# Performance work log

Measured on AMD Instinct MI355X. Metric: run time of the kernel, lower is better.

Reference implementation:

```python
import jax, jax.numpy as jnp
import numpy as np

B, SEQ, D, H, E = 4, 4096, 1024, 4096, 8
CAPACITY = 2.0  # k = int(S * capacity) token-expert slots


def setup_inputs() -> dict:
    key = jax.random.key(0)
    ks = jax.random.split(key, 5)
    x = jax.random.normal(ks[0], (B, SEQ, D), dtype=jnp.float32)
    gate_weight = jax.random.normal(ks[1], (E, D), dtype=jnp.float32) * 0.006
    expert_bias = jnp.ones((E, 1), dtype=jnp.float32)
    W1 = jax.random.normal(ks[2], (E, D, H), dtype=jnp.float32) * 0.02
    b1 = jnp.zeros((E, H), dtype=jnp.float32)
    W2 = jax.random.normal(ks[3], (E, H, D), dtype=jnp.float32) * 0.02
    b2 = jnp.zeros((E, D), dtype=jnp.float32)
    return {"x": x, "gate_weight": gate_weight, "expert_bias": expert_bias,
            "W1": W1, "b1": b1, "W2": W2, "b2": b2}


def reference(x, gate_weight, expert_bias, W1, b1, W2, b2):
    Bv, s, Dv = x.shape
    xf = x.reshape(-1, Dv)               # [S, D]
    S = xf.shape[0]
    k = int(S * CAPACITY)

    # router: bias_sigmoid -> scores[e, s] = sigmoid(x @ gate.T + bias)
    logits = jnp.einsum('sd,ed->es', xf, gate_weight) + expert_bias  # [E, S]
    scores = jax.nn.sigmoid(logits)

    # global top-k over flattened (E*S) token-expert pairs
    value, index = jax.lax.top_k(scores.reshape(-1), k)
    index_expert = index // S
    index_token = index % S

    # combine weights: gating score at selected slots, 0 elsewhere (topk indices unique)
    C = jnp.zeros((E * S,), dtype=scores.dtype).at[index].set(value).reshape(E, S)

    token_each_expert = jax.ops.segment_sum(
        jnp.ones((k,), dtype=jnp.float32), index_expert, num_segments=E) / float(k)

    # per-expert MLP, gated combine (tokens with C==0 contribute exactly 0,
    # matching the torch gather/MLP/index_add_ path)
    out = jnp.zeros_like(xf)
    for e in range(E):
        h = jax.nn.gelu(xf @ W1[e] + b1[e], approximate=True)  # [S, H]
        y = h @ W2[e] + b2[e]                                  # [S, D]
        out = out + C[e][:, None] * y

    x_out = out.reshape(Bv, s, Dv)
    return x_out, token_each_expert, jnp.ones((E,), dtype=scores.dtype)
```

## Files before the change

kernel.cpp:

```cpp
#include <hip/hip_runtime.h>
#include <hip/hip_bf16.h>
#include <cstdint>
#include <cstdio>
#include <math.h>

#define S_TOK 16384
#define E_EXP 8
#define DDIM  1024
#define HDIM  4096
#define K_SEL 32768
#define ES    131072
#define OUT_XO 16777216

#define WS_META    0x000000u
#define WS_HIST    0x000100u
#define WS_COUNTS  0x001100u
#define WS_EXOFF   0x001200u
#define WS_TIEIDX  0x001300u
#define WS_CLEAR   0x00A000u
#define WS_TOK     0x010000u
#define WS_COEF    0x090000u
#define WS_SCORES  0x110000u
#define WS_TCNT    0x190000u
#define WS_TSLOT   0x1A0000u
#define WS_XB      0x400000u
#define WS_W1T    0x2400000u
#define WS_W2T    0x6400000u
#define WS_HBUF   0xA400000u
#define WS_TOTAL  0x1A400000u
#define WS_YBUF   WS_W1T

typedef __attribute__((ext_vector_type(4))) float f32x4;
typedef __attribute__((ext_vector_type(8))) short bf16x8;

__device__ __forceinline__ void gload_lds16(const void* g, void* l) {
  __builtin_amdgcn_global_load_lds((const __attribute__((address_space(1))) void*)g,
                                   (__attribute__((address_space(3))) void*)l, 16, 0, 0);
}

__device__ __forceinline__ float gelu_f(float x) {
  float u = __builtin_fmaf(x * x * x, 0.044715f, x);
  float e = __builtin_amdgcn_exp2f(-2.302207976f * u);
  return x * __builtin_amdgcn_rcpf(1.0f + e);
}

#define ABUF0 0
#define ABUF1 32768
#define BBUF0 65536
#define BBUF1 98304
#define HALF  16384

#define PH_BAR() __builtin_amdgcn_s_barrier()
#define VMC0M()  asm volatile("s_waitcnt vmcnt(0)" ::: "memory")
#define VMCN(N)  asm volatile("s_waitcnt vmcnt(" #N ")" ::: "memory")

#define STAGE_A(DST, KE) do { \
  gload_lds16(aS00 + (KE), lds + (DST) + w * 2048); \
  gload_lds16(aS01 + (KE), lds + (DST) + w * 2048 + 1024); \
  gload_lds16(aS10 + (KE), lds + (DST) + HALF + w * 2048); \
  gload_lds16(aS11 + (KE), lds + (DST) + HALF + w * 2048 + 1024); } while (0)
#define STAGE_B(DST, KE) do { \
  gload_lds16(bS00 + (KE), lds + (DST) + w * 2048); \
  gload_lds16(bS01 + (KE), lds + (DST) + w * 2048 + 1024); \
  gload_lds16(bS10 + (KE), lds + (DST) + HALF + w * 2048); \
  gload_lds16(bS11 + (KE), lds + (DST) + HALF + w * 2048 + 1024); } while (0)

#define LDS_A03(AB) { _Pragma("unroll") for (int ii = 0; ii < 4; ii++) { \
  a03[ii][0] = *(const bf16x8*)(lds + (AB) + arow + ii * 2048 + pc0); \
  a03[ii][1] = *(const bf16x8*)(lds + (AB) + arow + ii * 2048 + pc1); } }
#define LDS_A47(AB) { _Pragma("unroll") for (int ii = 0; ii < 4; ii++) { \
  a47[ii][0] = *(const bf16x8*)(lds + (AB) + arow + (4 + ii) * 2048 + pc0); \
  a47[ii][1] = *(const bf16x8*)(lds + (AB) + arow + (4 + ii) * 2048 + pc1); } }
#define LDS_B01(BB) { _Pragma("unroll") for (int jj = 0; jj < 2; jj++) { \
  b01[jj][0] = *(const bf16x8*)(lds + (BB) + brow + jj * 2048 + pc0); \
  b01[jj][1] = *(const bf16x8*)(lds + (BB) + brow + jj * 2048 + pc1); } }
#define LDS_B23(BB) { _Pragma("unroll") for (int jj = 0; jj < 2; jj++) { \
  b23[jj][0] = *(const bf16x8*)(lds + (BB) + brow + (2 + jj) * 2048 + pc0); \
  b23[jj][1] = *(const bf16x8*)(lds + (BB) + brow + (2 + jj) * 2048 + pc1); } }

#define MF(AA, BF, IL, JL) { _Pragma("unroll") for (int ii = 0; ii < 4; ii++) \
  _Pragma("unroll") for (int jj = 0; jj < 2; jj++) { \
    acc[(IL)+ii][(JL)+jj] = __builtin_amdgcn_mfma_f32_16x16x32_bf16(AA[ii][0], BF[jj][0], acc[(IL)+ii][(JL)+jj], 0, 0, 0); \
    acc[(IL)+ii][(JL)+jj] = __builtin_amdgcn_mfma_f32_16x16x32_bf16(AA[ii][1], BF[jj][1], acc[(IL)+ii][(JL)+jj], 0, 0, 0); } }

#define TILE(T, AB, BB, ABn, BBn, STGA, STGB, NB, NA) do { \
  PH_BAR(); \
  LDS_A03(AB); \
  if (STGA) STAGE_A(ABn, ((T) + 1) * 64); \
  __builtin_amdgcn_s_setprio(1); MF(a03, b01, 0, 0); MF(a03, b23, 0, 2); __builtin_amdgcn_s_setprio(0); \
  PH_BAR(); \
  LDS_A47(AB); \
  if (STGB) STAGE_B(BB, ((T) + 2) * 64); \
  __builtin_amdgcn_s_setprio(1); MF(a47, b01, 4, 0); __builtin_amdgcn_s_setprio(0); \
  VMCN(NB); \
  LDS_B01(BBn); \
  __builtin_amdgcn_s_setprio(1); MF(a47, b23, 4, 2); __builtin_amdgcn_s_setprio(0); \
  LDS_B23(BBn); \
  VMCN(NA); \
} while (0)

#define TILE_LAST(AB, BB) do { \
  PH_BAR(); \
  LDS_A03(AB); \
  __builtin_amdgcn_s_setprio(1); MF(a03, b01, 0, 0); MF(a03, b23, 0, 2); __builtin_amdgcn_s_setprio(0); \
  PH_BAR(); \
  LDS_A47(AB); \
  __builtin_amdgcn_s_setprio(1); MF(a47, b01, 4, 0); MF(a47, b23, 4, 2); __builtin_amdgcn_s_setprio(0); \
} while (0)

__global__ __launch_bounds__(256) void transpose_bf16_kernel(
    const float* __restrict__ in, __hip_bfloat16* __restrict__ outp, int R, int C)
{
  __shared__ __hip_bfloat16 t[64][66];
  const int c0 = blockIdx.x * 64, r0 = blockIdx.y * 64;
  const size_t eoff = (size_t)blockIdx.z * (size_t)R * (size_t)C;
  const int tx = threadIdx.x & 15, ty = threadIdx.x >> 4;
  const float* ip = in + eoff + (size_t)r0 * C + c0;
#pragma unroll
  for (int i = 0; i < 4; i++) {
    const int r = ty + i * 16;
    float4 v = *(const float4*)(ip + (size_t)r * C + tx * 4);
    t[r][tx * 4 + 0] = __float2bfloat16(v.x);
    t[r][tx * 4 + 1] = __float2bfloat16(v.y);
    t[r][tx * 4 + 2] = __float2bfloat16(v.z);
    t[r][tx * 4 + 3] = __float2bfloat16(v.w);
  }
  __syncthreads();
  __hip_bfloat16* op = outp + eoff + (size_t)c0 * R + r0;
#pragma unroll
  for (int i = 0; i < 4; i++) {
    const int c = ty + i * 16;
    ushort4 u;
    u.x = *(const unsigned short*)&t[tx * 4 + 0][c];
    u.y = *(const unsigned short*)&t[tx * 4 + 1][c];
    u.z = *(const unsigned short*)&t[tx * 4 + 2][c];
    u.w = *(const unsigned short*)&t[tx * 4 + 3][c];
    *(ushort4*)(op + (size_t)c * R + tx * 4) = u;
  }
}

__global__ __launch_bounds__(256) void router_kernel(
    const float* __restrict__ x, const float* __restrict__ gw, const float* __restrict__ bias,
    float* __restrict__ scores, __hip_bfloat16* __restrict__ xb, unsigned* __restrict__ hist0)
{
  __shared__ float g[E_EXP * DDIM];
  __shared__ float bs[E_EXP];
  __shared__ unsigned h0[256];
  const int tid = threadIdx.x;
  for (int i = tid; i < E_EXP * DDIM; i += 256) g[i] = gw[i];
  if (tid < E_EXP) bs[tid] = bias[tid];
  h0[tid] = 0;
  __syncthreads();
  const int w = tid >> 6, lane = tid & 63;
  const int s = blockIdx.x * 4 + w;
  double acc[E_EXP] = {0, 0, 0, 0, 0, 0, 0, 0};
  const float* xrow = x + (size_t)s * DDIM;
  __hip_bfloat16* xbrow = xb + (size_t)s * DDIM;
#pragma unroll 4
  for (int j = 0; j < 16; j++) {
    int d = lane + 64 * j;
    float xv = xrow[d];
    xbrow[d] = __float2bfloat16(xv);
#pragma unroll
    for (int e = 0; e < E_EXP; e++) acc[e] += (double)xv * (double)g[e * DDIM + d];
  }
#pragma unroll
  for (int e = 0; e < E_EXP; e++) {
    double a = acc[e];
#pragma unroll
    for (int off = 32; off > 0; off >>= 1) a += __shfl_xor(a, off);
    acc[e] = a;
  }
  if (lane == 0) {
#pragma unroll
    for (int e = 0; e < E_EXP; e++) {
      double lg = acc[e] + (double)bs[e];
      float sc = (float)(1.0 / (1.0 + exp(-lg)));
      scores[(size_t)e * S_TOK + s] = sc;
      atomicAdd(&h0[__float_as_uint(sc) >> 24], 1u);
    }
  }
  __syncthreads();
  if (h0[tid]) atomicAdd(&hist0[tid], h0[tid]);
}

__global__ __launch_bounds__(256) void hist_pass_kernel(
    const float* __restrict__ scores, const unsigned* __restrict__ meta,
    unsigned* __restrict__ hist, int pass)
{
  __shared__ unsigned h[256];
  const int tid = threadIdx.x;
  h[tid] = 0;
  __syncthreads();
  const unsigned prefix = meta[0];
  const int pshift = 32 - 8 * pass;
  const int bshift = 24 - 8 * pass;
  const unsigned base = blockIdx.x * 2048 + tid;
#pragma unroll
  for (int i = 0; i < 8; i++) {
    unsigned b = __float_as_uint(scores[base + i * 256]);
    bool ok = ((b >> pshift) == prefix);
    if (ok) atomicAdd(&h[(b >> bshift) & 0xFFu], 1u);
  }
  __syncthreads();
  if (h[tid]) atomicAdd(&hist[tid], h[tid]);
}

__global__ __launch_bounds__(256) void scan_pass_kernel(
    const unsigned* __restrict__ hist, unsigned* __restrict__ meta, int final)
{
  const int t = threadIdx.x;
  const unsigned v = hist[t];
  const unsigned prefix = meta[0];
  const unsigned above = meta[1];
  __shared__ unsigned csum[256];
  csum[t] = v;
  __syncthreads();
  for (int off = 1; off < 256; off <<= 1) {
    unsigned add = (t + off < 256) ? csum[t + off] : 0u;
    __syncthreads();
    csum[t] += add;
    __syncthreads();
  }
  const unsigned cge = csum[t];
  const unsigned cgt = cge - v;
  if (above + cgt < K_SEL && above + cge >= K_SEL) {
    meta[0] = (prefix << 8) | (unsigned)t;
    meta[1] = above + cgt;
    if (final) {
      meta[2] = (prefix << 8) | (unsigned)t;
      meta[4] = K_SEL - (above + cgt);
    }
  }
}

__global__ __launch_bounds__(256) void sel_kernel(const float* __restrict__ scores,
                                                  unsigned* __restrict__ meta,
                                                  unsigned* __restrict__ counts,
                                                  int* __restrict__ tok_list,
                                                  float* __restrict__ coef_list,
                                                  unsigned* __restrict__ tie_idx,
                                                  unsigned* __restrict__ tcnt,
                                                  unsigned* __restrict__ tslot)
{
  __shared__ unsigned lcnt[E_EXP], lbase[E_EXP];
  const int tid = threadIdx.x;
  if (tid < E_EXP) lcnt[tid] = 0;
  __syncthreads();
  const unsigned i = blockIdx.x * 256 + tid;
  const float v = scores[i];
  const unsigned b = __float_as_uint(v);
  const unsigned t = meta[2];
  const bool sel = (b > t);
  const unsigned e = i >> 14;
  unsigned myslot = 0;
  if (sel) myslot = atomicAdd(&lcnt[e], 1u);
  else if (b == t) {
    unsigned ts = atomicAdd(&meta[5], 1u);
    if (ts < 8192u) tie_idx[ts] = i;
  }
  __syncthreads();
  if (tid < E_EXP) lbase[tid] = atomicAdd(&counts[tid], lcnt[tid]);
  __syncthreads();
  if (sel) {
    const unsigned slot = lbase[e] + myslot;
    const unsigned p = e * S_TOK + slot;
    const unsigned tok = i & 16383u;
    tok_list[p] = (int)tok;
    coef_list[p] = v;
    unsigned us = atomicAdd(&tcnt[tok], 1u);
    tslot[tok * 8u + us] = (e << 14) | slot;
  }
}

__global__ __launch_bounds__(256) void fin_kernel(const unsigned* __restrict__ meta,
                                                  const unsigned* __restrict__ tie_idx,
                                                  unsigned* __restrict__ counts,
                                                  int* __restrict__ tok_list,
                                                  float* __restrict__ coef_list,
                                                  unsigned* __restrict__ tcnt,
                                                  unsigned* __restrict__ tslot,
                                                  unsigned* __restrict__ exoff,
                                                  float* __restrict__ tail)
{
  unsigned tcnt_ties = meta[5]; if (tcnt_ties > 8192u) tcnt_ties = 8192u;
  const unsigned q = meta[4];
  const float tval = __uint_as_float(meta[2]);
  for (unsigned t = threadIdx.x; t < tcnt_ties; t += 256) {
    unsigned idx = tie_idx[t];
    unsigned rank = 0;
    for (unsigned u = 0; u < tcnt_ties; u++) rank += (tie_idx[u] < idx) ? 1u : 0u;
    if (rank < q) {
      const unsigned e = idx >> 14;
      const unsigned tok = idx & 16383u;
      const unsigned slot = atomicAdd(&counts[e], 1u);
      tok_list[e * S_TOK + slot] = (int)tok;
      coef_list[e * S_TOK + slot] = tval;
      unsigned us = atomicAdd(&tcnt[tok], 1u);
      tslot[tok * 8u + us] = (e << 14) | slot;
    }
  }
  __syncthreads();
  if (threadIdx.x == 0) {
    unsigned o = 0;
    for (int e = 0; e < E_EXP; e++) { exoff[e] = o; o += counts[e]; }
    exoff[E_EXP] = o;
  }
  if (threadIdx.x < E_EXP) {
    tail[threadIdx.x] = (float)counts[threadIdx.x] * (1.0f / (float)K_SEL);
    tail[E_EXP + threadIdx.x] = 1.0f;
  }
}

__global__ __launch_bounds__(512, 1) void gemm1_kernel(
    const __hip_bfloat16* __restrict__ xb,
    const __hip_bfloat16* __restrict__ w1t,
    const float* __restrict__ b1,
    const int* __restrict__ tok_list,
    const unsigned* __restrict__ counts,
    const unsigned* __restrict__ exoff,
    __hip_bfloat16* __restrict__ hbuf)
{
  const int id = blockIdx.x;
  const int L = (id & 7) * 1024 + (id >> 3);
  const int e = L >> 10;
  const int rem = L & 1023;
  const int cnt = (int)counts[e];
  const int m0 = (rem >> 4) * 256;
  if (m0 >= cnt) return;
  const int n0 = (rem & 15) * 256;

  __shared__ __align__(16) char lds[131072];
  __shared__ int s_tok[256];

  const int tid = threadIdx.x;
  const int w = tid >> 6, lane = tid & 63;
  const int wm = w >> 2, wn = w & 3;

  if (tid < 256) {
    int mi = m0 + tid;
    s_tok[tid] = tok_list[e * S_TOK + (mi < cnt ? mi : cnt - 1)];
  }
  __syncthreads();

  const int srl0 = w * 16 + (lane >> 3);
  const int srl1 = srl0 + 8;
  const int gch = ((lane & 7) ^ (lane >> 3)) * 8;
  const __hip_bfloat16* aS00 = xb + (size_t)s_tok[srl0] * DDIM + gch;
  const __hip_bfloat16* aS01 = xb + (size_t)s_tok[srl1] * DDIM + gch;
  const __hip_bfloat16* aS10 = xb + (size_t)s_tok[128 + srl0] * DDIM + gch;
  const __hip_bfloat16* aS11 = xb + (size_t)s_tok[128 + srl1] * DDIM + gch;
  const __hip_bfloat16* w1e = w1t + (size_t)e * HDIM * DDIM;
  const __hip_bfloat16* bS00 = w1e + (size_t)(n0 + srl0) * DDIM + gch;
  const __hip_bfloat16* bS01 = w1e + (size_t)(n0 + srl1) * DDIM + gch;
  const __hip_bfloat16* bS10 = w1e + (size_t)(n0 + 128 + srl0) * DDIM + gch;
  const __hip_bfloat16* bS11 = w1e + (size_t)(n0 + 128 + srl1) * DDIM + gch;

  const int arow = (wm * 128 + (lane & 15)) * 128;
  const int brow = (wn * 64 + (lane & 15)) * 128;
  const int pc0 = (((lane >> 4)) ^ (lane & 7)) * 16;
  const int pc1 = (((lane >> 4) + 4) ^ (lane & 7)) * 16;

  f32x4 acc[8][4] = {};
  bf16x8 a03[4][2], a47[4][2], b01[2][2], b23[2][2];

  STAGE_A(ABUF0, 0);
  STAGE_B(BBUF0, 0);
  STAGE_B(BBUF1, 64);
  VMC0M();
  PH_BAR();
  LDS_B01(BBUF0); LDS_B23(BBUF0);

  const int NKT = DDIM / 64;
  int kt = 0;
  for (; kt + 2 < NKT; kt += 2) {
    TILE(kt,     ABUF0, BBUF0, ABUF1, BBUF1, true, true, 8, 4);
    TILE(kt + 1, ABUF1, BBUF1, ABUF0, BBUF0, true, true, 8, 4);
  }
  TILE(kt, ABUF0, BBUF0, ABUF1, BBUF1, true, false, 4, 0);
  TILE_LAST(ABUF1, BBUF1);
  __syncthreads();

  __hip_bfloat16* stg = (__hip_bfloat16*)lds;
  const float* b1e = b1 + (size_t)e * HDIM;
  float bvj[4];
#pragma unroll
  for (int j = 0; j < 4; j++) bvj[j] = b1e[n0 + wn * 64 + j * 16 + (lane & 15)];
  const int pbase = (int)exoff[e] + m0;

#pragma unroll
  for (int P = 0; P < 4; P++) {
    __syncthreads();
    if (wm == (P >> 1)) {
      const int ib = (P & 1) * 4;
#pragma unroll
      for (int ii = 0; ii < 4; ii++)
#pragma unroll
        for (int jj = 0; jj < 4; jj++)
#pragma unroll
          for (int r = 0; r < 4; r++) {
            const int rloc = ii * 16 + (lane >> 4) * 4 + r;
            const int col = wn * 64 + jj * 16 + (lane & 15);
            stg[rloc * 264 + col] = __float2bfloat16(gelu_f(acc[ib + ii][jj][r] + bvj[jj]));
          }
    }
    __syncthreads();
    const int rr = tid >> 3;
    const int m = P * 64 + rr;
    if (m0 + m < cnt) {
      __hip_bfloat16* dst = hbuf + (size_t)(pbase + m) * HDIM + n0;
      const __hip_bfloat16* src = stg + rr * 264;
#pragma unroll
      for (int c = 0; c < 4; c++)
        *(uint4*)(dst + (tid & 7) * 8 + c * 64) = *(const uint4*)(src + (tid & 7) * 8 + c * 64);
    }
  }
}

__global__ __launch_bounds__(512, 1) void gemm2_kernel(
    const __hip_bfloat16* __restrict__ hbuf,
    const __hip_bfloat16* __restrict__ w2t,
    const float* __restrict__ b2,
    const float* __restrict__ coef_list,
    const unsigned* __restrict__ counts,
    const unsigned* __restrict__ exoff,
    __hip_bfloat16* __restrict__ ybuf)
{
  const int id = blockIdx.x;
  const int L = (id & 7) * 256 + (id >> 3);
  const int e = L >> 8;
  const int rem = L & 255;
  const int cnt = (int)counts[e];
  const int m0 = (rem >> 2) * 256;
  if (m0 >= cnt) return;
  const int n0 = (rem & 3) * 256;

  __shared__ __align__(16) char lds[131072];
  __shared__ float s_coef[256];

  const int tid = threadIdx.x;
  const int w = tid >> 6, lane = tid & 63;
  const int wm = w >> 2, wn = w & 3;
  const int pb = (int)exoff[e];

  if (tid < 256) {
    int mi = m0 + tid;
    s_coef[tid] = (mi < cnt) ? coef_list[e * S_TOK + mi] : 0.0f;
  }
  __syncthreads();

  const int srl0 = w * 16 + (lane >> 3);
  const int srl1 = srl0 + 8;
  const int gch = ((lane & 7) ^ (lane >> 3)) * 8;
  const int ra0 = pb + ((m0 + srl0 < cnt) ? m0 + srl0 : cnt - 1);
  const int ra1 = pb + ((m0 + srl1 < cnt) ? m0 + srl1 : cnt - 1);
  const int ra2 = pb + ((m0 + 128 + srl0 < cnt) ? m0 + 128 + srl0 : cnt - 1);
  const int ra3 = pb + ((m0 + 128 + srl1 < cnt) ? m0 + 128 + srl1 : cnt - 1);
  const __hip_bfloat16* aS00 = hbuf + (size_t)ra0 * HDIM + gch;
  const __hip_bfloat16* aS01 = hbuf + (size_t)ra1 * HDIM + gch;
  const __hip_bfloat16* aS10 = hbuf + (size_t)ra2 * HDIM + gch;
  const __hip_bfloat16* aS11 = hbuf + (size_t)ra3 * HDIM + gch;
  const __hip_bfloat16* w2e = w2t + (size_t)e * DDIM * HDIM;
  const __hip_bfloat16* bS00 = w2e + (size_t)(n0 + srl0) * HDIM + gch;
  const __hip_bfloat16* bS01 = w2e + (size_t)(n0 + srl1) * HDIM + gch;
  const __hip_bfloat16* bS10 = w2e + (size_t)(n0 + 128 + srl0) * HDIM + gch;
  const __hip_bfloat16* bS11 = w2e + (size_t)(n0 + 128 + srl1) * HDIM + gch;

  const int arow = (wm * 128 + (lane & 15)) * 128;
  const int brow = (wn * 64 + (lane & 15)) * 128;
  const int pc0 = (((lane >> 4)) ^ (lane & 7)) * 16;
  const int pc1 = (((lane >> 4) + 4) ^ (lane & 7)) * 16;

  f32x4 acc[8][4] = {};
  bf16x8 a03[4][2], a47[4][2], b01[2][2], b23[2][2];

  STAGE_A(ABUF0, 0);
  STAGE_B(BBUF0, 0);
  STAGE_B(BBUF1, 64);
  VMC0M();
  PH_BAR();
  LDS_B01(BBUF0); LDS_B23(BBUF0);

  const int NKT = HDIM / 64;
  int kt = 0;
  for (; kt + 2 < NKT; kt += 2) {
    TILE(kt,     ABUF0, BBUF0, ABUF1, BBUF1, true, true, 8, 4);
    TILE(kt + 1, ABUF1, BBUF1, ABUF0, BBUF0, true, true, 8, 4);
  }
  TILE(kt, ABUF0, BBUF0, ABUF1, BBUF1, true, false, 4, 0);
  TILE_LAST(ABUF1, BBUF1);
  __syncthreads();

  __hip_bfloat16* stg = (__hip_bfloat16*)lds;
  const float* b2e = b2 + (size_t)e * DDIM;
  float bvj[4];
#pragma unroll
  for (int j = 0; j < 4; j++) bvj[j] = b2e[n0 + wn * 64 + j * 16 + (lane & 15)];
  const int pbase = pb + m0;

#pragma unroll
  for (int P = 0; P < 4; P++) {
    __syncthreads();
    if (wm == (P >> 1)) {
      const int ib = (P & 1) * 4;
#pragma unroll
      for (int ii = 0; ii < 4; ii++)
#pragma unroll
        for (int jj = 0; jj < 4; jj++)
#pragma unroll
          for (int r = 0; r < 4; r++) {
            const int rloc = ii * 16 + (lane >> 4) * 4 + r;
            const int col = wn * 64 + jj * 16 + (lane & 15);
            const float cf = s_coef[P * 64 + rloc];
            stg[rloc * 264 + col] = __float2bfloat16(cf * (acc[ib + ii][jj][r] + bvj[jj]));
          }
    }
    __syncthreads();
    const int rr = tid >> 3;
    const int m = P * 64 + rr;
    if (m0 + m < cnt) {
      __hip_bfloat16* dst = ybuf + (size_t)(pbase + m) * DDIM + n0;
      const __hip_bfloat16* src = stg + rr * 264;
#pragma unroll
      for (int c = 0; c < 4; c++)
        *(uint4*)(dst + (tid & 7) * 8 + c * 64) = *(const uint4*)(src + (tid & 7) * 8 + c * 64);
    }
  }
}

__global__ __launch_bounds__(256) void combine_kernel(
    const __hip_bfloat16* __restrict__ ybuf,
    const unsigned* __restrict__ tcnt,
    const unsigned* __restrict__ tslot,
    const unsigned* __restrict__ exoff,
    float* __restrict__ out)
{
  const int tid = threadIdx.x;
  const int t = blockIdx.x * 2 + (tid >> 7);
  const int d0 = (tid & 127) * 8;
  float a[8] = {0, 0, 0, 0, 0, 0, 0, 0};
  const unsigned n = tcnt[t];
  for (unsigned s = 0; s < n; s++) {
    const unsigned code = tslot[t * 8u + s];
    const unsigned p = exoff[code >> 14] + (code & 16383u);
    bf16x8 v = *(const bf16x8*)(ybuf + (size_t)p * DDIM + d0);
#pragma unroll
    for (int k = 0; k < 8; k++)
      a[k] += __uint_as_float(((unsigned)(unsigned short)v[k]) << 16);
  }
  float* op = out + (size_t)t * DDIM + d0;
  *(float4*)op = make_float4(a[0], a[1], a[2], a[3]);
  *(float4*)(op + 4) = make_float4(a[4], a[5], a[6], a[7]);
}

extern "C" void kernel_launch(void* const* d_in, const int* in_sizes, int n_in,
                              void* d_out, int out_size, void* d_ws, size_t ws_size,
                              hipStream_t stream) {
  const float* x    = (const float*)d_in[0];
  const float* gw   = (const float*)d_in[1];
  const float* bias = (const float*)d_in[2];
  const float* W1   = (const float*)d_in[3];
  const float* b1   = (const float*)d_in[4];
  const float* W2   = (const float*)d_in[5];
  const float* b2   = (const float*)d_in[6];
  float* out = (float*)d_out;
  char* ws = (char*)d_ws;

  if (ws_size < (size_t)WS_TOTAL) {
    fprintf(stderr, "kernel_launch: ws_size %zu < required %u\n", ws_size, WS_TOTAL);
    return;
  }

  unsigned* meta   = (unsigned*)(ws + WS_META);
  unsigned* hist   = (unsigned*)(ws + WS_HIST);
  unsigned* counts = (unsigned*)(ws + WS_COUNTS);
  unsigned* exoff  = (unsigned*)(ws + WS_EXOFF);
  unsigned* tiei   = (unsigned*)(ws + WS_TIEIDX);
  unsigned* tcnt   = (unsigned*)(ws + WS_TCNT);
  unsigned* tslot  = (unsigned*)(ws + WS_TSLOT);
  int*      tokl   = (int*)(ws + WS_TOK);
  float*    coefl  = (float*)(ws + WS_COEF);
  float*    scores = (float*)(ws + WS_SCORES);
  __hip_bfloat16* xb   = (__hip_bfloat16*)(ws + WS_XB);
  __hip_bfloat16* w1t  = (__hip_bfloat16*)(ws + WS_W1T);
  __hip_bfloat16* w2t  = (__hip_bfloat16*)(ws + WS_W2T);
  __hip_bfloat16* hbuf = (__hip_bfloat16*)(ws + WS_HBUF);
  __hip_bfloat16* ybuf = (__hip_bfloat16*)(ws + WS_YBUF);

  hipMemsetAsync(ws, 0, WS_CLEAR, stream);
  hipMemsetAsync(ws + WS_TCNT, 0, S_TOK * sizeof(unsigned), stream);

  transpose_bf16_kernel<<<dim3(HDIM / 64, DDIM / 64, E_EXP), 256, 0, stream>>>(W1, w1t, DDIM, HDIM);
  transpose_bf16_kernel<<<dim3(DDIM / 64, HDIM / 64, E_EXP), 256, 0, stream>>>(W2, w2t, HDIM, DDIM);

  router_kernel<<<S_TOK / 4, 256, 0, stream>>>(x, gw, bias, scores, xb, hist);

  scan_pass_kernel<<<1, 256, 0, stream>>>(hist, meta, 0);
  for (int p = 1; p < 4; p++) {
    hist_pass_kernel<<<ES / 2048, 256, 0, stream>>>(scores, meta, hist + p * 256, p);
    scan_pass_kernel<<<1, 256, 0, stream>>>(hist + p * 256, meta, p == 3);
  }
  sel_kernel<<<ES / 256, 256, 0, stream>>>(scores, meta, counts, tokl, coefl, tiei, tcnt, tslot);
  fin_kernel<<<1, 256, 0, stream>>>(meta, tiei, counts, tokl, coefl, tcnt, tslot, exoff, out + OUT_XO);

  gemm1_kernel<<<8192, 512, 0, stream>>>(xb, w1t, b1, tokl, counts, exoff, hbuf);
  gemm2_kernel<<<2048, 512, 0, stream>>>(hbuf, w2t, b2, coefl, counts, exoff, ybuf);
  combine_kernel<<<S_TOK / 2, 256, 0, stream>>>(ybuf, tcnt, tslot, exoff, out);
}
```

Before: 866.0 us.

## Restructure GEMM k-loop into barrier-synchronised LDS/MFMA phases with explicit lgkm waits

Replaces the per-tile LDS-read/MFMA interleave in both expert GEMMs with a four-phase schedule. Each phase issues its LDS fragment reads, waits on lgkmcnt, and runs an MFMA quadrant between workgroup barriers. B fragments are now read from the current buffer inside the tile instead of prefetched from the next one, and the prologue no longer waits for all global loads. The goal is tighter overlap of LDS traffic and global-to-LDS staging with matrix work across waves. The cost is more barriers per k-tile and LDS reads that are less hidden behind MFMAs.

```diff
diff --git a/kernel.cpp b/kernel.cpp
--- a/kernel.cpp
+++ b/kernel.cpp
@@ -51,8 +51,11 @@
 #define HALF  16384
 
 #define PH_BAR() __builtin_amdgcn_s_barrier()
-#define VMC0M()  asm volatile("s_waitcnt vmcnt(0)" ::: "memory")
+#define SP1()    __builtin_amdgcn_s_setprio(1)
+#define SP0()    __builtin_amdgcn_s_setprio(0)
 #define VMCN(N)  asm volatile("s_waitcnt vmcnt(" #N ")" ::: "memory")
+#define LGK0()   do { asm volatile("s_waitcnt lgkmcnt(0)" ::: "memory"); __builtin_amdgcn_sched_barrier(0); } while (0)
+#define LGK8()   asm volatile("s_waitcnt lgkmcnt(8)")
 
 #define STAGE_A(DST, KE) do { \
   gload_lds16(aS00 + (KE), lds + (DST) + w * 2048); \
@@ -83,29 +86,44 @@
     acc[(IL)+ii][(JL)+jj] = __builtin_amdgcn_mfma_f32_16x16x32_bf16(AA[ii][0], BF[jj][0], acc[(IL)+ii][(JL)+jj], 0, 0, 0); \
     acc[(IL)+ii][(JL)+jj] = __builtin_amdgcn_mfma_f32_16x16x32_bf16(AA[ii][1], BF[jj][1], acc[(IL)+ii][(JL)+jj], 0, 0, 0); } }
 
-#define TILE(T, AB, BB, ABn, BBn, STGA, STGB, NB, NA) do { \
+#define KG8(T, AB, BB, ABn, STGA, STGB, NV) do { \
+   \
+  LDS_A03(AB); LDS_B01(BB); \
+  if (STGA) STAGE_A(ABn, ((T) + 1) * 64); \
+  LGK8(); \
+  PH_BAR(); LGK0(); \
+  SP1(); MF(a03, b01, 0, 0); SP0(); \
   PH_BAR(); \
-  LDS_A03(AB); \
-  if (STGA) STAGE_A(ABn, ((T) + 1) * 64); \
-  __builtin_amdgcn_s_setprio(1); MF(a03, b01, 0, 0); MF(a03, b23, 0, 2); __builtin_amdgcn_s_setprio(0); \
+   \
+  LDS_B23(BB); \
+  PH_BAR(); LGK0(); \
+  SP1(); MF(a03, b23, 0, 2); SP0(); \
+  PH_BAR(); \
+   \
+  LDS_A47(AB); \
+  if (STGB) STAGE_B(BB, ((T) + 2) * 64); \
+  PH_BAR(); LGK0(); \
+  SP1(); MF(a47, b23, 4, 2); SP0(); \
+  PH_BAR(); \
+   \
+  VMCN(NV); \
+  PH_BAR(); \
+  SP1(); MF(a47, b01, 4, 0); SP0(); \
+  PH_BAR(); \
+} while (0)
+
+#define KG8_LAST(AB, BB) do { \
+  LDS_A03(AB); LDS_B01(BB); \
+  PH_BAR(); LGK0(); \
+  SP1(); MF(a03, b01, 0, 0); SP0(); \
+  PH_BAR(); \
+  LDS_B23(BB); \
+  PH_BAR(); LGK0(); \
+  SP1(); MF(a03, b23, 0, 2); SP0(); \
   PH_BAR(); \
   LDS_A47(AB); \
-  if (STGB) STAGE_B(BB, ((T) + 2) * 64); \
-  __builtin_amdgcn_s_setprio(1); MF(a47, b01, 4, 0); __builtin_amdgcn_s_setprio(0); \
-  VMCN(NB); \
-  LDS_B01(BBn); \
-  __builtin_amdgcn_s_setprio(1); MF(a47, b23, 4, 2); __builtin_amdgcn_s_setprio(0); \
-  LDS_B23(BBn); \
-  VMCN(NA); \
-} while (0)
-
-#define TILE_LAST(AB, BB) do { \
-  PH_BAR(); \
-  LDS_A03(AB); \
-  __builtin_amdgcn_s_setprio(1); MF(a03, b01, 0, 0); MF(a03, b23, 0, 2); __builtin_amdgcn_s_setprio(0); \
-  PH_BAR(); \
-  LDS_A47(AB); \
-  __builtin_amdgcn_s_setprio(1); MF(a47, b01, 4, 0); MF(a47, b23, 4, 2); __builtin_amdgcn_s_setprio(0); \
+  PH_BAR(); LGK0(); \
+  SP1(); MF(a47, b23, 4, 2); MF(a47, b01, 4, 0); SP0(); \
 } while (0)
 
 __global__ __launch_bounds__(256) void transpose_bf16_kernel(
@@ -367,18 +385,17 @@
   STAGE_A(ABUF0, 0);
   STAGE_B(BBUF0, 0);
   STAGE_B(BBUF1, 64);
-  VMC0M();
+  VMCN(4);
   PH_BAR();
-  LDS_B01(BBUF0); LDS_B23(BBUF0);
 
   const int NKT = DDIM / 64;
   int kt = 0;
   for (; kt + 2 < NKT; kt += 2) {
-    TILE(kt,     ABUF0, BBUF0, ABUF1, BBUF1, true, true, 8, 4);
-    TILE(kt + 1, ABUF1, BBUF1, ABUF0, BBUF0, true, true, 8, 4);
-  }
-  TILE(kt, ABUF0, BBUF0, ABUF1, BBUF1, true, false, 4, 0);
-  TILE_LAST(ABUF1, BBUF1);
+    KG8(kt,     ABUF0, BBUF0, ABUF1, true, true, 4);
+    KG8(kt + 1, ABUF1, BBUF1, ABUF0, true, true, 4);
+  }
+  KG8(kt, ABUF0, BBUF0, ABUF1, true, false, 0);
+  KG8_LAST(ABUF1, BBUF1);
   __syncthreads();
 
   __hip_bfloat16* stg = (__hip_bfloat16*)lds;
@@ -477,18 +494,17 @@
   STAGE_A(ABUF0, 0);
   STAGE_B(BBUF0, 0);
   STAGE_B(BBUF1, 64);
-  VMC0M();
+  VMCN(4);
   PH_BAR();
-  LDS_B01(BBUF0); LDS_B23(BBUF0);
 
   const int NKT = HDIM / 64;
   int kt = 0;
   for (; kt + 2 < NKT; kt += 2) {
-    TILE(kt,     ABUF0, BBUF0, ABUF1, BBUF1, true, true, 8, 4);
-    TILE(kt + 1, ABUF1, BBUF1, ABUF0, BBUF0, true, true, 8, 4);
-  }
-  TILE(kt, ABUF0, BBUF0, ABUF1, BBUF1, true, false, 4, 0);
-  TILE_LAST(ABUF1, BBUF1);
+    KG8(kt,     ABUF0, BBUF0, ABUF1, true, true, 4);
+    KG8(kt + 1, ABUF1, BBUF1, ABUF0, true, true, 4);
+  }
+  KG8(kt, ABUF0, BBUF0, ABUF1, true, false, 0);
+  KG8_LAST(ABUF1, BBUF1);
   __syncthreads();
 
   __hip_bfloat16* stg = (__hip_bfloat16*)lds;
```

After: 915.2 us. +5.7%, slower.

## Shrink expert GEMM tiles to 128x128 with 256-thread blocks, two per CU

Applied to the files above, without the earlier changes.

Both expert GEMM kernels move from 256x256 tiles with 8 waves and 128KB of LDS to 128x128 tiles with 4 waves and 64KB of LDS, so two blocks can be resident per CU. The grids grow four-fold, and the staging, fragment loads, wait counts and epilogue are rewritten to match. The aim is better occupancy and finer load balance on the ragged per-expert token counts, where partially filled 256-row tiles waste work. The cost is lower arithmetic intensity, meaning more global and LDS traffic per FLOP, plus more blocks re-reading the weights.

```diff
diff --git a/kernel.cpp b/kernel.cpp
--- a/kernel.cpp
+++ b/kernel.cpp
@@ -45,32 +45,31 @@
 }
 
 #define ABUF0 0
-#define ABUF1 32768
-#define BBUF0 65536
-#define BBUF1 98304
-#define HALF  16384
+#define ABUF1 16384
+#define BBUF0 32768
+#define BBUF1 49152
 
 #define PH_BAR() __builtin_amdgcn_s_barrier()
 #define VMC0M()  asm volatile("s_waitcnt vmcnt(0)" ::: "memory")
 #define VMCN(N)  asm volatile("s_waitcnt vmcnt(" #N ")" ::: "memory")
 
 #define STAGE_A(DST, KE) do { \
-  gload_lds16(aS00 + (KE), lds + (DST) + w * 2048); \
-  gload_lds16(aS01 + (KE), lds + (DST) + w * 2048 + 1024); \
-  gload_lds16(aS10 + (KE), lds + (DST) + HALF + w * 2048); \
-  gload_lds16(aS11 + (KE), lds + (DST) + HALF + w * 2048 + 1024); } while (0)
+  gload_lds16(aS0 + (KE), lds + (DST) + w * 1024); \
+  gload_lds16(aS1 + (KE), lds + (DST) + 4096 + w * 1024); \
+  gload_lds16(aS2 + (KE), lds + (DST) + 8192 + w * 1024); \
+  gload_lds16(aS3 + (KE), lds + (DST) + 12288 + w * 1024); } while (0)
 #define STAGE_B(DST, KE) do { \
-  gload_lds16(bS00 + (KE), lds + (DST) + w * 2048); \
-  gload_lds16(bS01 + (KE), lds + (DST) + w * 2048 + 1024); \
-  gload_lds16(bS10 + (KE), lds + (DST) + HALF + w * 2048); \
-  gload_lds16(bS11 + (KE), lds + (DST) + HALF + w * 2048 + 1024); } while (0)
-
-#define LDS_A03(AB) { _Pragma("unroll") for (int ii = 0; ii < 4; ii++) { \
-  a03[ii][0] = *(const bf16x8*)(lds + (AB) + arow + ii * 2048 + pc0); \
-  a03[ii][1] = *(const bf16x8*)(lds + (AB) + arow + ii * 2048 + pc1); } }
-#define LDS_A47(AB) { _Pragma("unroll") for (int ii = 0; ii < 4; ii++) { \
-  a47[ii][0] = *(const bf16x8*)(lds + (AB) + arow + (4 + ii) * 2048 + pc0); \
-  a47[ii][1] = *(const bf16x8*)(lds + (AB) + arow + (4 + ii) * 2048 + pc1); } }
+  gload_lds16(bS0 + (KE), lds + (DST) + w * 1024); \
+  gload_lds16(bS1 + (KE), lds + (DST) + 4096 + w * 1024); \
+  gload_lds16(bS2 + (KE), lds + (DST) + 8192 + w * 1024); \
+  gload_lds16(bS3 + (KE), lds + (DST) + 12288 + w * 1024); } while (0)
+
+#define LDS_A01(AB) { _Pragma("unroll") for (int ii = 0; ii < 2; ii++) { \
+  a01[ii][0] = *(const bf16x8*)(lds + (AB) + arow + ii * 2048 + pc0); \
+  a01[ii][1] = *(const bf16x8*)(lds + (AB) + arow + ii * 2048 + pc1); } }
+#define LDS_A23(AB) { _Pragma("unroll") for (int ii = 0; ii < 2; ii++) { \
+  a23[ii][0] = *(const bf16x8*)(lds + (AB) + arow + (2 + ii) * 2048 + pc0); \
+  a23[ii][1] = *(const bf16x8*)(lds + (AB) + arow + (2 + ii) * 2048 + pc1); } }
 #define LDS_B01(BB) { _Pragma("unroll") for (int jj = 0; jj < 2; jj++) { \
   b01[jj][0] = *(const bf16x8*)(lds + (BB) + brow + jj * 2048 + pc0); \
   b01[jj][1] = *(const bf16x8*)(lds + (BB) + brow + jj * 2048 + pc1); } }
@@ -78,34 +77,34 @@
   b23[jj][0] = *(const bf16x8*)(lds + (BB) + brow + (2 + jj) * 2048 + pc0); \
   b23[jj][1] = *(const bf16x8*)(lds + (BB) + brow + (2 + jj) * 2048 + pc1); } }
 
-#define MF(AA, BF, IL, JL) { _Pragma("unroll") for (int ii = 0; ii < 4; ii++) \
+#define MF(AA, BF, IL, JL) { _Pragma("unroll") for (int ii = 0; ii < 2; ii++) \
   _Pragma("unroll") for (int jj = 0; jj < 2; jj++) { \
     acc[(IL)+ii][(JL)+jj] = __builtin_amdgcn_mfma_f32_16x16x32_bf16(AA[ii][0], BF[jj][0], acc[(IL)+ii][(JL)+jj], 0, 0, 0); \
     acc[(IL)+ii][(JL)+jj] = __builtin_amdgcn_mfma_f32_16x16x32_bf16(AA[ii][1], BF[jj][1], acc[(IL)+ii][(JL)+jj], 0, 0, 0); } }
 
 #define TILE(T, AB, BB, ABn, BBn, STGA, STGB, NB, NA) do { \
   PH_BAR(); \
-  LDS_A03(AB); \
+  LDS_A01(AB); \
   if (STGA) STAGE_A(ABn, ((T) + 1) * 64); \
-  __builtin_amdgcn_s_setprio(1); MF(a03, b01, 0, 0); MF(a03, b23, 0, 2); __builtin_amdgcn_s_setprio(0); \
+  __builtin_amdgcn_s_setprio(1); MF(a01, b01, 0, 0); MF(a01, b23, 0, 2); __builtin_amdgcn_s_setprio(0); \
+  VMCN(NB); \
   PH_BAR(); \
-  LDS_A47(AB); \
+  LDS_A23(AB); \
   if (STGB) STAGE_B(BB, ((T) + 2) * 64); \
-  __builtin_amdgcn_s_setprio(1); MF(a47, b01, 4, 0); __builtin_amdgcn_s_setprio(0); \
-  VMCN(NB); \
+  __builtin_amdgcn_s_setprio(1); MF(a23, b01, 2, 0); __builtin_amdgcn_s_setprio(0); \
   LDS_B01(BBn); \
-  __builtin_amdgcn_s_setprio(1); MF(a47, b23, 4, 2); __builtin_amdgcn_s_setprio(0); \
+  __builtin_amdgcn_s_setprio(1); MF(a23, b23, 2, 2); __builtin_amdgcn_s_setprio(0); \
   LDS_B23(BBn); \
   VMCN(NA); \
 } while (0)
 
 #define TILE_LAST(AB, BB) do { \
   PH_BAR(); \
-  LDS_A03(AB); \
-  __builtin_amdgcn_s_setprio(1); MF(a03, b01, 0, 0); MF(a03, b23, 0, 2); __builtin_amdgcn_s_setprio(0); \
+  LDS_A01(AB); \
+  __builtin_amdgcn_s_setprio(1); MF(a01, b01, 0, 0); MF(a01, b23, 0, 2); __builtin_amdgcn_s_setprio(0); \
   PH_BAR(); \
-  LDS_A47(AB); \
-  __builtin_amdgcn_s_setprio(1); MF(a47, b01, 4, 0); MF(a47, b23, 4, 2); __builtin_amdgcn_s_setprio(0); \
+  LDS_A23(AB); \
+  __builtin_amdgcn_s_setprio(1); MF(a23, b01, 2, 0); MF(a23, b23, 2, 2); __builtin_amdgcn_s_setprio(0); \
 } while (0)
 
 __global__ __launch_bounds__(256) void transpose_bf16_kernel(
@@ -312,7 +311,7 @@
   }
 }
 
-__global__ __launch_bounds__(512, 1) void gemm1_kernel(
+__global__ __launch_bounds__(256, 2) void gemm1_kernel(
     const __hip_bfloat16* __restrict__ xb,
     const __hip_bfloat16* __restrict__ w1t,
     const float* __restrict__ b1,
@@ -322,47 +321,46 @@
     __hip_bfloat16* __restrict__ hbuf)
 {
   const int id = blockIdx.x;
-  const int L = (id & 7) * 1024 + (id >> 3);
-  const int e = L >> 10;
-  const int rem = L & 1023;
+  const int L = (id & 7) * 4096 + (id >> 3);
+  const int e = L >> 12;
+  const int rem = L & 4095;
   const int cnt = (int)counts[e];
-  const int m0 = (rem >> 4) * 256;
+  const int m0 = (rem >> 5) * 128;
   if (m0 >= cnt) return;
-  const int n0 = (rem & 15) * 256;
-
-  __shared__ __align__(16) char lds[131072];
-  __shared__ int s_tok[256];
+  const int n0 = (rem & 31) * 128;
+
+  __shared__ __align__(16) char lds[65536];
+  __shared__ int s_tok[128];
 
   const int tid = threadIdx.x;
   const int w = tid >> 6, lane = tid & 63;
-  const int wm = w >> 2, wn = w & 3;
-
-  if (tid < 256) {
+  const int wm = w >> 1, wn = w & 1;
+
+  if (tid < 128) {
     int mi = m0 + tid;
     s_tok[tid] = tok_list[e * S_TOK + (mi < cnt ? mi : cnt - 1)];
   }
   __syncthreads();
 
-  const int srl0 = w * 16 + (lane >> 3);
-  const int srl1 = srl0 + 8;
+  const int srl = w * 8 + (lane >> 3);
   const int gch = ((lane & 7) ^ (lane >> 3)) * 8;
-  const __hip_bfloat16* aS00 = xb + (size_t)s_tok[srl0] * DDIM + gch;
-  const __hip_bfloat16* aS01 = xb + (size_t)s_tok[srl1] * DDIM + gch;
-  const __hip_bfloat16* aS10 = xb + (size_t)s_tok[128 + srl0] * DDIM + gch;
-  const __hip_bfloat16* aS11 = xb + (size_t)s_tok[128 + srl1] * DDIM + gch;
+  const __hip_bfloat16* aS0 = xb + (size_t)s_tok[srl] * DDIM + gch;
+  const __hip_bfloat16* aS1 = xb + (size_t)s_tok[srl + 32] * DDIM + gch;
+  const __hip_bfloat16* aS2 = xb + (size_t)s_tok[srl + 64] * DDIM + gch;
+  const __hip_bfloat16* aS3 = xb + (size_t)s_tok[srl + 96] * DDIM + gch;
   const __hip_bfloat16* w1e = w1t + (size_t)e * HDIM * DDIM;
-  const __hip_bfloat16* bS00 = w1e + (size_t)(n0 + srl0) * DDIM + gch;
-  const __hip_bfloat16* bS01 = w1e + (size_t)(n0 + srl1) * DDIM + gch;
-  const __hip_bfloat16* bS10 = w1e + (size_t)(n0 + 128 + srl0) * DDIM + gch;
-  const __hip_bfloat16* bS11 = w1e + (size_t)(n0 + 128 + srl1) * DDIM + gch;
-
-  const int arow = (wm * 128 + (lane & 15)) * 128;
+  const __hip_bfloat16* bS0 = w1e + (size_t)(n0 + srl) * DDIM + gch;
+  const __hip_bfloat16* bS1 = w1e + (size_t)(n0 + srl + 32) * DDIM + gch;
+  const __hip_bfloat16* bS2 = w1e + (size_t)(n0 + srl + 64) * DDIM + gch;
+  const __hip_bfloat16* bS3 = w1e + (size_t)(n0 + srl + 96) * DDIM + gch;
+
+  const int arow = (wm * 64 + (lane & 15)) * 128;
   const int brow = (wn * 64 + (lane & 15)) * 128;
   const int pc0 = (((lane >> 4)) ^ (lane & 7)) * 16;
   const int pc1 = (((lane >> 4) + 4) ^ (lane & 7)) * 16;
 
-  f32x4 acc[8][4] = {};
-  bf16x8 a03[4][2], a47[4][2], b01[2][2], b23[2][2];
+  f32x4 acc[4][4] = {};
+  bf16x8 a01[2][2], a23[2][2], b01[2][2], b23[2][2];
 
   STAGE_A(ABUF0, 0);
   STAGE_B(BBUF0, 0);
@@ -374,8 +372,8 @@
   const int NKT = DDIM / 64;
   int kt = 0;
   for (; kt + 2 < NKT; kt += 2) {
-    TILE(kt,     ABUF0, BBUF0, ABUF1, BBUF1, true, true, 8, 4);
-    TILE(kt + 1, ABUF1, BBUF1, ABUF0, BBUF0, true, true, 8, 4);
+    TILE(kt,     ABUF0, BBUF0, ABUF1, BBUF1, true, true, 4, 4);
+    TILE(kt + 1, ABUF1, BBUF1, ABUF0, BBUF0, true, true, 4, 4);
   }
   TILE(kt, ABUF0, BBUF0, ABUF1, BBUF1, true, false, 4, 0);
   TILE_LAST(ABUF1, BBUF1);
@@ -389,10 +387,9 @@
   const int pbase = (int)exoff[e] + m0;
 
 #pragma unroll
-  for (int P = 0; P < 4; P++) {
+  for (int P = 0; P < 2; P++) {
     __syncthreads();
-    if (wm == (P >> 1)) {
-      const int ib = (P & 1) * 4;
+    if (wm == P) {
 #pragma unroll
       for (int ii = 0; ii < 4; ii++)
 #pragma unroll
@@ -401,23 +398,24 @@
           for (int r = 0; r < 4; r++) {
             const int rloc = ii * 16 + (lane >> 4) * 4 + r;
             const int col = wn * 64 + jj * 16 + (lane & 15);
-            stg[rloc * 264 + col] = __float2bfloat16(gelu_f(acc[ib + ii][jj][r] + bvj[jj]));
+            stg[rloc * 136 + col] = __float2bfloat16(gelu_f(acc[ii][jj][r] + bvj[jj]));
           }
     }
     __syncthreads();
-    const int rr = tid >> 3;
+    const int rr = tid >> 2;
+    const int chb = (tid & 3) * 8;
     const int m = P * 64 + rr;
     if (m0 + m < cnt) {
       __hip_bfloat16* dst = hbuf + (size_t)(pbase + m) * HDIM + n0;
-      const __hip_bfloat16* src = stg + rr * 264;
+      const __hip_bfloat16* src = stg + rr * 136;
 #pragma unroll
       for (int c = 0; c < 4; c++)
-        *(uint4*)(dst + (tid & 7) * 8 + c * 64) = *(const uint4*)(src + (tid & 7) * 8 + c * 64);
+        *(uint4*)(dst + chb + c * 32) = *(const uint4*)(src + chb + c * 32);
     }
   }
 }
 
-__global__ __launch_bounds__(512, 1) void gemm2_kernel(
+__global__ __launch_bounds__(256, 2) void gemm2_kernel(
     const __hip_bfloat16* __restrict__ hbuf,
     const __hip_bfloat16* __restrict__ w2t,
     const float* __restrict__ b2,
@@ -427,52 +425,51 @@
     __hip_bfloat16* __restrict__ ybuf)
 {
   const int id = blockIdx.x;
-  const int L = (id & 7) * 256 + (id >> 3);
-  const int e = L >> 8;
-  const int rem = L & 255;
+  const int L = (id & 7) * 1024 + (id >> 3);
+  const int e = L >> 10;
+  const int rem = L & 1023;
   const int cnt = (int)counts[e];
-  const int m0 = (rem >> 2) * 256;
+  const int m0 = (rem >> 3) * 128;
   if (m0 >= cnt) return;
-  const int n0 = (rem & 3) * 256;
-
-  __shared__ __align__(16) char lds[131072];
-  __shared__ float s_coef[256];
+  const int n0 = (rem & 7) * 128;
+
+  __shared__ __align__(16) char lds[65536];
+  __shared__ float s_coef[128];
 
   const int tid = threadIdx.x;
   const int w = tid >> 6, lane = tid & 63;
-  const int wm = w >> 2, wn = w & 3;
+  const int wm = w >> 1, wn = w & 1;
   const int pb = (int)exoff[e];
 
-  if (tid < 256) {
+  if (tid < 128) {
     int mi = m0 + tid;
     s_coef[tid] = (mi < cnt) ? coef_list[e * S_TOK + mi] : 0.0f;
   }
   __syncthreads();
 
-  const int srl0 = w * 16 + (lane >> 3);
-  const int srl1 = srl0 + 8;
+  const int srl = w * 8 + (lane >> 3);
   const int gch = ((lane & 7) ^ (lane >> 3)) * 8;
-  const int ra0 = pb + ((m0 + srl0 < cnt) ? m0 + srl0 : cnt - 1);
-  const int ra1 = pb + ((m0 + srl1 < cnt) ? m0 + srl1 : cnt - 1);
-  const int ra2 = pb + ((m0 + 128 + srl0 < cnt) ? m0 + 128 + srl0 : cnt - 1);
-  const int ra3 = pb + ((m0 + 128 + srl1 < cnt) ? m0 + 128 + srl1 : cnt - 1);
-  const __hip_bfloat16* aS00 = hbuf + (size_t)ra0 * HDIM + gch;
-  const __hip_bfloat16* aS01 = hbuf + (size_t)ra1 * HDIM + gch;
-  const __hip_bfloat16* aS10 = hbuf + (size_t)ra2 * HDIM + gch;
-  const __hip_bfloat16* aS11 = hbuf + (size_t)ra3 * HDIM + gch;
+  const int ra0 = pb + ((m0 + srl < cnt) ? m0 + srl : cnt - 1);
+  const int ra1 = pb + ((m0 + srl + 32 < cnt) ? m0 + srl + 32 : cnt - 1);
+  const int ra2 = pb + ((m0 + srl + 64 < cnt) ? m0 + srl + 64 : cnt - 1);
+  const int ra3 = pb + ((m0 + srl + 96 < cnt) ? m0 + srl + 96 : cnt - 1);
+  const __hip_bfloat16* aS0 = hbuf + (size_t)ra0 * HDIM + gch;
+  const __hip_bfloat16* aS1 = hbuf + (size_t)ra1 * HDIM + gch;
+  const __hip_bfloat16* aS2 = hbuf + (size_t)ra2 * HDIM + gch;
+  const __hip_bfloat16* aS3 = hbuf + (size_t)ra3 * HDIM + gch;
   const __hip_bfloat16* w2e = w2t + (size_t)e * DDIM * HDIM;
-  const __hip_bfloat16* bS00 = w2e + (size_t)(n0 + srl0) * HDIM + gch;
-  const __hip_bfloat16* bS01 = w2e + (size_t)(n0 + srl1) * HDIM + gch;
-  const __hip_bfloat16* bS10 = w2e + (size_t)(n0 + 128 + srl0) * HDIM + gch;
-  const __hip_bfloat16* bS11 = w2e + (size_t)(n0 + 128 + srl1) * HDIM + gch;
-
-  const int arow = (wm * 128 + (lane & 15)) * 128;
+  const __hip_bfloat16* bS0 = w2e + (size_t)(n0 + srl) * HDIM + gch;
+  const __hip_bfloat16* bS1 = w2e + (size_t)(n0 + srl + 32) * HDIM + gch;
+  const __hip_bfloat16* bS2 = w2e + (size_t)(n0 + srl + 64) * HDIM + gch;
+  const __hip_bfloat16* bS3 = w2e + (size_t)(n0 + srl + 96) * HDIM + gch;
+
+  const int arow = (wm * 64 + (lane & 15)) * 128;
   const int brow = (wn * 64 + (lane & 15)) * 128;
   const int pc0 = (((lane >> 4)) ^ (lane & 7)) * 16;
   const int pc1 = (((lane >> 4) + 4) ^ (lane & 7)) * 16;
 
-  f32x4 acc[8][4] = {};
-  bf16x8 a03[4][2], a47[4][2], b01[2][2], b23[2][2];
+  f32x4 acc[4][4] = {};
+  bf16x8 a01[2][2], a23[2][2], b01[2][2], b23[2][2];
 
   STAGE_A(ABUF0, 0);
   STAGE_B(BBUF0, 0);
@@ -484,8 +481,8 @@
   const int NKT = HDIM / 64;
   int kt = 0;
   for (; kt + 2 < NKT; kt += 2) {
-    TILE(kt,     ABUF0, BBUF0, ABUF1, BBUF1, true, true, 8, 4);
-    TILE(kt + 1, ABUF1, BBUF1, ABUF0, BBUF0, true, true, 8, 4);
+    TILE(kt,     ABUF0, BBUF0, ABUF1, BBUF1, true, true, 4, 4);
+    TILE(kt + 1, ABUF1, BBUF1, ABUF0, BBUF0, true, true, 4, 4);
   }
   TILE(kt, ABUF0, BBUF0, ABUF1, BBUF1, true, false, 4, 0);
   TILE_LAST(ABUF1, BBUF1);
@@ -499,10 +496,9 @@
   const int pbase = pb + m0;
 
 #pragma unroll
-  for (int P = 0; P < 4; P++) {
+  for (int P = 0; P < 2; P++) {
     __syncthreads();
-    if (wm == (P >> 1)) {
-      const int ib = (P & 1) * 4;
+    if (wm == P) {
 #pragma unroll
       for (int ii = 0; ii < 4; ii++)
 #pragma unroll
@@ -512,18 +508,19 @@
             const int rloc = ii * 16 + (lane >> 4) * 4 + r;
             const int col = wn * 64 + jj * 16 + (lane & 15);
             const float cf = s_coef[P * 64 + rloc];
-            stg[rloc * 264 + col] = __float2bfloat16(cf * (acc[ib + ii][jj][r] + bvj[jj]));
+            stg[rloc * 136 + col] = __float2bfloat16(cf * (acc[ii][jj][r] + bvj[jj]));
           }
     }
     __syncthreads();
-    const int rr = tid >> 3;
+    const int rr = tid >> 2;
+    const int chb = (tid & 3) * 8;
     const int m = P * 64 + rr;
     if (m0 + m < cnt) {
       __hip_bfloat16* dst = ybuf + (size_t)(pbase + m) * DDIM + n0;
-      const __hip_bfloat16* src = stg + rr * 264;
+      const __hip_bfloat16* src = stg + rr * 136;
 #pragma unroll
       for (int c = 0; c < 4; c++)
-        *(uint4*)(dst + (tid & 7) * 8 + c * 64) = *(const uint4*)(src + (tid & 7) * 8 + c * 64);
+        *(uint4*)(dst + chb + c * 32) = *(const uint4*)(src + chb + c * 32);
     }
   }
 }
@@ -603,7 +600,7 @@
   sel_kernel<<<ES / 256, 256, 0, stream>>>(scores, meta, counts, tokl, coefl, tiei, tcnt, tslot);
   fin_kernel<<<1, 256, 0, stream>>>(meta, tiei, counts, tokl, coefl, tcnt, tslot, exoff, out + OUT_XO);
 
-  gemm1_kernel<<<8192, 512, 0, stream>>>(xb, w1t, b1, tokl, counts, exoff, hbuf);
-  gemm2_kernel<<<2048, 512, 0, stream>>>(hbuf, w2t, b2, coefl, counts, exoff, ybuf);
+  gemm1_kernel<<<32768, 256, 0, stream>>>(xb, w1t, b1, tokl, counts, exoff, hbuf);
+  gemm2_kernel<<<8192, 256, 0, stream>>>(hbuf, w2t, b2, coefl, counts, exoff, ybuf);
   combine_kernel<<<S_TOK / 2, 256, 0, stream>>>(ybuf, tcnt, tslot, exoff, out);
 }
```

Result: slower. 922.5 us (+6.5%).
